# Performance work log

Hardware: AMD Instinct MI355X
Metric: run time of the kernel (lower is better)

Reference implementation:

```python
import jax, jax.numpy as jnp
import numpy as np

DIM = 512
NUM_HEADS = 8
HEAD_DIM = DIM // NUM_HEADS
KERNEL = (3, 5, 5)  # (kd, kh, kw), must be odd and <= spatial dims
B, D, H, W = 1, 6, 48, 96


def setup_inputs() -> dict:
    key = jax.random.key(0)
    ks = jax.random.split(key, 5)
    x = jax.random.normal(ks[0], (B, D, H, W, DIM), jnp.float32)
    w_qkv = jax.random.normal(ks[1], (DIM, 3 * DIM), jnp.float32) * 0.02
    b_qkv = jax.random.normal(ks[2], (3 * DIM,), jnp.float32) * 0.02
    w_proj = jax.random.normal(ks[3], (DIM, DIM), jnp.float32) * 0.02
    b_proj = jax.random.normal(ks[4], (DIM,), jnp.float32) * 0.02
    return {"x": x, "w_qkv": w_qkv, "b_qkv": b_qkv, "w_proj": w_proj, "b_proj": b_proj}


def _nbhd_idx(L, k):
    # NATTEN neighborhood: window of exactly k keys, centered, shifted inward at edges.
    p = jnp.arange(L)
    start = jnp.clip(p - k // 2, 0, L - k)
    return start[:, None] + jnp.arange(k)[None, :]  # [L, k]


def _na3d(q, k, v, kernel):
    # q, k, v: [B, D, H, W, heads, hd]; q pre-scaled.
    kd, kh, kw = kernel
    _, Dd, Hh, Ww, _, _ = q.shape
    idx_d = _nbhd_idx(Dd, kd)
    idx_h = _nbhd_idx(Hh, kh)
    idx_w = _nbhd_idx(Ww, kw)
    offs = jnp.stack(
        jnp.meshgrid(jnp.arange(kd), jnp.arange(kh), jnp.arange(kw), indexing="ij"),
        axis=-1,
    ).reshape(-1, 3)  # [K3, 3]

    def shift(t, o):
        # gather the o-th neighbor of every query position along each spatial axis
        t = jnp.take(t, jnp.take(idx_d, o[0], axis=1), axis=1)
        t = jnp.take(t, jnp.take(idx_h, o[1], axis=1), axis=2)
        t = jnp.take(t, jnp.take(idx_w, o[2], axis=1), axis=3)
        return t

    def score_step(_, o):
        k_s = shift(k, o)
        s = jnp.einsum("bdhwnc,bdhwnc->bdhwn", q, k_s)
        return None, s

    _, scores = jax.lax.scan(score_step, None, offs)  # [K3, B, D, H, W, heads]
    attn = jax.nn.softmax(scores, axis=0)

    def out_step(acc, xs):
        o, a = xs
        v_s = shift(v, o)
        return acc + a[..., None] * v_s, None

    out, _ = jax.lax.scan(out_step, jnp.zeros_like(q), (offs, attn))
    return out


def reference(x, w_qkv, b_qkv, w_proj, b_proj):
    Bb, Dd, Hh, Ww, C = x.shape
    qkv = (x @ w_qkv + b_qkv).reshape(Bb, Dd, Hh, Ww, 3, NUM_HEADS, HEAD_DIM)
    q = qkv[..., 0, :, :]
    k = qkv[..., 1, :, :]
    v = qkv[..., 2, :, :]
    scale = HEAD_DIM ** (-0.5)
    # Faithful to source: module scales q by self.scale, then tuned_na3d applies
    # head_dim**-0.5 again inside the fused kernel -> net q * head_dim**-1.
    q = q * (scale * scale)
    out = _na3d(q, k, v, KERNEL).reshape(Bb, Dd, Hh, Ww, C)
    return out @ w_proj + b_proj
```

## Files before the change

kernel.cpp:

```cpp
#include <hip/hip_runtime.h>

#define DIMC   512
#define NHEADS 8
#define HDIM   64
#define DD     6
#define HHH    48
#define WWW    96
#define NPOS   (DD * HHH * WWW)

typedef unsigned short u16;
typedef __attribute__((ext_vector_type(8))) short bf16x8;
typedef __attribute__((ext_vector_type(4))) float f32x4;

static __device__ __forceinline__ float b2f(u16 u) {
    return __builtin_bit_cast(float, (unsigned)u << 16);
}
static __device__ __forceinline__ u16 f2b(float f) {
    unsigned x = __builtin_bit_cast(unsigned, f);
    return (u16)((x + 0x7fffu + ((x >> 16) & 1u)) >> 16);
}

static __device__ __forceinline__ void gload_lds16(const void* g, void* l) {
    __builtin_amdgcn_global_load_lds((const __attribute__((address_space(1))) void*)g,
                                     (__attribute__((address_space(3))) void*)l, 16, 0, 0);
}

__global__ __launch_bounds__(256) void cvt_all(
    const float* __restrict__ x, const float* __restrict__ w_qkv,
    const float* __restrict__ w_proj, u16* __restrict__ xb,
    u16* __restrict__ wqkvT, u16* __restrict__ wprojT)
{
    const int bid = blockIdx.x;
    const int tid = threadIdx.x;
    if (bid < 13824) {
        const int i = bid * 256 + tid;
        float4 v = reinterpret_cast<const float4*>(x)[i];
        ushort4 o = { f2b(v.x), f2b(v.y), f2b(v.z), f2b(v.w) };
        reinterpret_cast<ushort4*>(xb)[i] = o;
    } else if (bid < 13824 + 3072) {
        const int id = (bid - 13824) * 256 + tid;
        const int nn = id >> 9, kk = id & 511;
        wqkvT[id] = f2b(w_qkv[(size_t)kk * 1536 + nn]);
    } else {
        const int id = (bid - 16896) * 256 + tid;
        const int nn = id >> 9, kk = id & 511;
        wprojT[id] = f2b(w_proj[(size_t)kk * 512 + nn]);
    }
}

__global__ __launch_bounds__(512) void gemm_bf16_mfma(
    const u16* __restrict__ A, int lda,
    const u16* __restrict__ B, int ldb,
    const float* __restrict__ bias, int Kp,
    void* __restrict__ Cout, int ldc, int cmode, int nx)
{
    __shared__ u16 As[256 * 64];
    __shared__ u16 Bs[128 * 64];

    const int tid = threadIdx.x;
    const int l   = tid & 63;
    const int w   = tid >> 6;
    const int wr  = w >> 1;
    const int wc  = w & 1;

    const int cpx = gridDim.x >> 3;
    const int idp = (blockIdx.x & 7) * cpx + (blockIdx.x >> 3);
    const int by  = idp / nx;
    const int bx  = idp - by * nx;
    const int m0  = by * 256;
    const int n0  = bx * 128;

    const int lrow = l >> 3;
    const int swz  = ((l & 7) ^ lrow) * 8;
    const int arow = w * 32 + lrow;
    const int brow = w * 16 + lrow;

    const u16* ga = A + (size_t)(m0 + arow) * lda + swz;
    const u16* gb = B + (size_t)(n0 + brow) * ldb + swz;
    const size_t a8 = (size_t)8 * lda;
    const size_t b8 = (size_t)8 * ldb;
    u16* const la0 = As + w * 2048;
    u16* const lb0 = Bs + w * 1024;

    f32x4 acc[4][4];
#pragma unroll
    for (int i = 0; i < 4; i++)
#pragma unroll
        for (int j = 0; j < 4; j++) acc[i][j] = (f32x4)0.0f;

    const int c   = l & 15;
    const int g   = l >> 4;
    const int lk0 = ((0 * 4 + g) ^ (c & 7)) * 8;
    const int lk1 = ((1 * 4 + g) ^ (c & 7)) * 8;

#pragma unroll 1
    for (int k0 = 0; k0 < Kp; k0 += 64) {
#pragma unroll
        for (int q = 0; q < 4; ++q)
            gload_lds16(ga + q * a8, la0 + q * 512);
#pragma unroll
        for (int q = 0; q < 2; ++q)
            gload_lds16(gb + q * b8, lb0 + q * 512);
        ga += 64; gb += 64;
        __syncthreads();

        {
            bf16x8 af[4], bfr[4];
#pragma unroll
            for (int f = 0; f < 4; f++) {
                af[f]  = *reinterpret_cast<const bf16x8*>(&As[(wr * 64 + f * 16 + c) * 64 + lk0]);
                bfr[f] = *reinterpret_cast<const bf16x8*>(&Bs[(wc * 64 + f * 16 + c) * 64 + lk0]);
            }
#pragma unroll
            for (int i = 0; i < 4; i++)
#pragma unroll
                for (int j = 0; j < 4; j++)
                    acc[i][j] = __builtin_amdgcn_mfma_f32_16x16x32_bf16(af[i], bfr[j], acc[i][j], 0, 0, 0);
        }
        {
            bf16x8 af[4], bfr[4];
#pragma unroll
            for (int f = 0; f < 4; f++) {
                af[f]  = *reinterpret_cast<const bf16x8*>(&As[(wr * 64 + f * 16 + c) * 64 + lk1]);
                bfr[f] = *reinterpret_cast<const bf16x8*>(&Bs[(wc * 64 + f * 16 + c) * 64 + lk1]);
            }
#pragma unroll
            for (int i = 0; i < 4; i++)
#pragma unroll
                for (int j = 0; j < 4; j++)
                    acc[i][j] = __builtin_amdgcn_mfma_f32_16x16x32_bf16(af[i], bfr[j], acc[i][j], 0, 0, 0);
        }
        __syncthreads();
    }

#pragma unroll
    for (int i = 0; i < 4; i++) {
        const int mb = m0 + wr * 64 + i * 16 + g * 4;
#pragma unroll
        for (int j = 0; j < 4; j++) {
            const int n = n0 + wc * 64 + j * 16 + c;
            const float bv = bias[n];
            const float scn = (cmode && n < 512) ? 0.022542110f : 1.0f;
#pragma unroll
            for (int r = 0; r < 4; r++) {
                const float v = (acc[i][j][r] + bv) * scn;
                if (cmode) reinterpret_cast<u16*>(Cout)[(size_t)(mb + r) * ldc + n] = f2b(v);
                else       reinterpret_cast<float*>(Cout)[(size_t)(mb + r) * ldc + n] = v;
            }
        }
    }
}

__global__ __launch_bounds__(512, 4) void na3d_mfma(
    const u16* __restrict__ qkv, u16* __restrict__ attnc)
{
    __shared__ int   rowoff[192];
    __shared__ int   dlt[16];
    __shared__ u16   Vt[NHEADS][64][36];
    __shared__ float ssum_lds[NHEADS][16];

    const int bid = blockIdx.x;
    const int x   = bid & 7;
    const int u   = bid >> 3;
    const int twl = u / 72;
    const int r2  = u - twl * 72;
    const int pd  = r2 / 12;
    const int thp = r2 - pd * 12;
    const int h0  = thp * 4;
    const int w0  = (3 * x + twl) * 4;
    const int sd  = min(max(pd - 1, 0), DD - 3);
    const int shb = min(max(h0 - 2, 0), HHH - 5);
    const int swb = min(max(w0 - 2, 0), WWW - 5);

    const int tid = threadIdx.x;
    if (tid < 192) {
        const int dd = tid >> 6, hh = (tid >> 3) & 7, wu = tid & 7;
        const int row = (sd + dd) * (HHH * WWW)
                      + min(shb + hh, HHH - 1) * WWW + min(swb + wu, WWW - 1);
        rowoff[tid] = row * 1536;
    }
    if (tid < 16) {
        const int ph = h0 + (tid >> 2), pw = w0 + (tid & 3);
        const int dh = min(max(ph - 2, 0), HHH - 5) - shb;
        const int dw = min(max(pw - 2, 0), WWW - 5) - swb;
        dlt[tid] = (dh << 4) | dw;
    }
    __syncthreads();

    const int head = tid >> 6;
    const int l    = tid & 63;
    const int g    = l >> 4;
    const int c    = l & 15;

    const int qrowi = pd * (HHH * WWW) + (h0 + (c >> 2)) * WWW + (w0 + (c & 3));
    const u16* qrow = qkv + (size_t)qrowi * 1536 + head * HDIM;
    const bf16x8 qlo = *reinterpret_cast<const bf16x8*>(qrow + 8 * g);
    const bf16x8 qhi = *reinterpret_cast<const bf16x8*>(qrow + 32 + 8 * g);
    const int dparts = dlt[c];
    const int dh = dparts >> 4, dw = dparts & 15;

    f32x4 oacc[4];
#pragma unroll
    for (int j = 0; j < 4; j++) oacc[j] = (f32x4)0.0f;
    float ssum = 0.0f;

#pragma unroll 1
    for (int s = 0; s < 6; ++s) {
        {
            const int npair = l >> 2;
            const int chq   = l & 3;
#pragma unroll
            for (int rr = 0; rr < 2; ++rr) {
                const int ch8 = 8 * chq + 32 * rr;
                const int2 rp = *reinterpret_cast<const int2*>(&rowoff[s * 32 + 2 * npair]);
                const ushort4* pa = reinterpret_cast<const ushort4*>(qkv + rp.x + 1024 + head * HDIM + ch8);
                const ushort4* pb = reinterpret_cast<const ushort4*>(qkv + rp.y + 1024 + head * HDIM + ch8);
                ushort4 va0 = pa[0], va1 = pa[1];
                ushort4 vb0 = pb[0], vb1 = pb[1];
                const u16* va = reinterpret_cast<const u16*>(&va0);
                const u16* vb = reinterpret_cast<const u16*>(&vb0);
#pragma unroll
                for (int e = 0; e < 4; ++e) {
                    unsigned dwo = (unsigned)va[e] | ((unsigned)vb[e] << 16);
                    *reinterpret_cast<unsigned*>(&Vt[head][ch8 + e][2 * npair]) = dwo;
                }
                const u16* va2 = reinterpret_cast<const u16*>(&va1);
                const u16* vb2 = reinterpret_cast<const u16*>(&vb1);
#pragma unroll
                for (int e = 0; e < 4; ++e) {
                    unsigned dwo = (unsigned)va2[e] | ((unsigned)vb2[e] << 16);
                    *reinterpret_cast<unsigned*>(&Vt[head][ch8 + 4 + e][2 * npair]) = dwo;
                }
            }
        }

        unsigned pA, pB, pC, pD;
#pragma unroll
        for (int t = 0; t < 2; ++t) {
            const int sb0 = s * 32 + t * 16;
            const int ro  = rowoff[sb0 + c];
            const u16* kr = qkv + ro + 512 + head * HDIM;
            const bf16x8 klo = *reinterpret_cast<const bf16x8*>(kr + 8 * g);
            const bf16x8 khi = *reinterpret_cast<const bf16x8*>(kr + 32 + 8 * g);
            f32x4 sf = (f32x4)0.0f;
            sf = __builtin_amdgcn_mfma_f32_16x16x32_bf16(klo, qlo, sf, 0, 0, 0);
            sf = __builtin_amdgcn_mfma_f32_16x16x32_bf16(khi, qhi, sf, 0, 0, 0);
            const int sb  = sb0 + 4 * g;
            const int wu0 = sb & 7;
            const int hh_ = (sb >> 3) & 7;
            const bool hv = ((unsigned)(hh_ - dh) < 5u);
            float e0, e1, e2, e3;
            e0 = (hv && (unsigned)(wu0 + 0 - dw) < 5u) ? exp2f(sf[0]) : 0.0f;
            e1 = (hv && (unsigned)(wu0 + 1 - dw) < 5u) ? exp2f(sf[1]) : 0.0f;
            e2 = (hv && (unsigned)(wu0 + 2 - dw) < 5u) ? exp2f(sf[2]) : 0.0f;
            e3 = (hv && (unsigned)(wu0 + 3 - dw) < 5u) ? exp2f(sf[3]) : 0.0f;
            ssum += e0 + e1 + e2 + e3;
            const unsigned p01 = (unsigned)f2b(e0) | ((unsigned)f2b(e1) << 16);
            const unsigned p23 = (unsigned)f2b(e2) | ((unsigned)f2b(e3) << 16);
            if (t == 0) { pA = p01; pB = p23; }
            else        { pC = p01; pD = p23; }
        }

        asm volatile("v_permlane32_swap_b32 %0, %1" : "+v"(pA), "+v"(pC));
        asm volatile("v_permlane32_swap_b32 %0, %1" : "+v"(pB), "+v"(pD));
        asm volatile("v_permlane16_swap_b32 %0, %1" : "+v"(pA), "+v"(pC));
        asm volatile("v_permlane16_swap_b32 %0, %1" : "+v"(pB), "+v"(pD));

        {
            const int4 pv = make_int4((int)pA, (int)pB, (int)pC, (int)pD);
            const bf16x8 pfrag = __builtin_bit_cast(bf16x8, pv);
#pragma unroll
            for (int j = 0; j < 4; ++j) {
                const uint2 v01 = *reinterpret_cast<const uint2*>(&Vt[head][16 * j + c][8 * g]);
                const uint2 v23 = *reinterpret_cast<const uint2*>(&Vt[head][16 * j + c][8 * g + 4]);
                const int4 vv = make_int4((int)v01.x, (int)v01.y, (int)v23.x, (int)v23.y);
                const bf16x8 vfrag = __builtin_bit_cast(bf16x8, vv);
                oacc[j] = __builtin_amdgcn_mfma_f32_16x16x32_bf16(pfrag, vfrag, oacc[j], 0, 0, 0);
            }
        }
    }

    ssum += __shfl_xor(ssum, 16);
    ssum += __shfl_xor(ssum, 32);
    if (l < 16) ssum_lds[head][c] = ssum;
    const f32x4 sums4 = *reinterpret_cast<const f32x4*>(&ssum_lds[head][4 * g]);

    const int orow = pd * (HHH * WWW) + (h0 + g) * WWW + w0;
#pragma unroll
    for (int r = 0; r < 4; ++r) {
        const float inv = 1.0f / sums4[r];
        u16* base = attnc + (size_t)(orow + r) * 512 + head * HDIM;
#pragma unroll
        for (int j = 0; j < 4; ++j)
            base[16 * j + c] = f2b(oacc[j][r] * inv);
    }
}

extern "C" void kernel_launch(void* const* d_in, const int* in_sizes, int n_in,
                              void* d_out, int out_size, void* d_ws, size_t ws_size,
                              hipStream_t stream)
{
    const float* x      = (const float*)d_in[0];
    const float* w_qkv  = (const float*)d_in[1];
    const float* b_qkv  = (const float*)d_in[2];
    const float* w_proj = (const float*)d_in[3];
    const float* b_proj = (const float*)d_in[4];
    float* out = (float*)d_out;

    u16* qkvb   = (u16*)d_ws;
    u16* attnc  = qkvb  + (size_t)NPOS * 1536;
    u16* xb     = attnc + (size_t)NPOS * 512;
    u16* wqkvT  = xb    + (size_t)NPOS * 512;
    u16* wprojT = wqkvT + (size_t)1536 * 512;

    cvt_all<<<17920, 256, 0, stream>>>(x, w_qkv, w_proj, xb, wqkvT, wprojT);

    gemm_bf16_mfma<<<(NPOS / 256) * (1536 / 128), 512, 0, stream>>>(
        xb, 512, wqkvT, 512, b_qkv, 512, qkvb, 1536, 1, 1536 / 128);

    na3d_mfma<<<NPOS / 16, 512, 0, stream>>>(qkvb, attnc);

    gemm_bf16_mfma<<<(NPOS / 256) * (512 / 128), 512, 0, stream>>>(
        attnc, 512, wprojT, 512, b_proj, 512, out, 512, 0, 512 / 128);
}
```

Before: 162.1 us.

## Process two depth slices per attention block to share K/V neighborhood loads

Each neighborhood-attention block now handles a 4x4 query tile across two adjacent depth slices. It loads a 4-deep K/V halo once and applies per-slice depth masks, where before each block loaded a 3-deep halo for a single slice. This cuts redundant K/V global loads and V transposes into LDS per output, and halves the grid size. In exchange each block does more MFMA work per loaded tile, computes some masked-out scores, and holds more accumulator registers, which may lower occupancy.

```diff
diff --git a/kernel.cpp b/kernel.cpp
--- a/kernel.cpp
+++ b/kernel.cpp
@@ -154,28 +154,30 @@
 __global__ __launch_bounds__(512, 4) void na3d_mfma(
     const u16* __restrict__ qkv, u16* __restrict__ attnc)
 {
-    __shared__ int   rowoff[192];
+    __shared__ int   rowoff[256];
     __shared__ int   dlt[16];
     __shared__ u16   Vt[NHEADS][64][36];
-    __shared__ float ssum_lds[NHEADS][16];
+    __shared__ float ssum_lds[NHEADS][2][16];
 
     const int bid = blockIdx.x;
     const int x   = bid & 7;
     const int u   = bid >> 3;
-    const int twl = u / 72;
-    const int r2  = u - twl * 72;
-    const int pd  = r2 / 12;
-    const int thp = r2 - pd * 12;
+    const int twl = u / 36;
+    const int r2  = u - twl * 36;
+    const int d0  = r2 / 12;
+    const int thp = r2 - d0 * 12;
     const int h0  = thp * 4;
     const int w0  = (3 * x + twl) * 4;
-    const int sd  = min(max(pd - 1, 0), DD - 3);
+    const int sdu = min(max(2 * d0 - 1, 0), DD - 4);
     const int shb = min(max(h0 - 2, 0), HHH - 5);
     const int swb = min(max(w0 - 2, 0), WWW - 5);
+    const int ddlt0 = min(max(2 * d0 - 1, 0), DD - 3) - sdu;
+    const int ddlt1 = min(max(2 * d0, 0), DD - 3) - sdu;
 
     const int tid = threadIdx.x;
-    if (tid < 192) {
+    if (tid < 256) {
         const int dd = tid >> 6, hh = (tid >> 3) & 7, wu = tid & 7;
-        const int row = (sd + dd) * (HHH * WWW)
+        const int row = (sdu + dd) * (HHH * WWW)
                       + min(shb + hh, HHH - 1) * WWW + min(swb + wu, WWW - 1);
         rowoff[tid] = row * 1536;
     }
@@ -192,20 +194,23 @@
     const int g    = l >> 4;
     const int c    = l & 15;
 
-    const int qrowi = pd * (HHH * WWW) + (h0 + (c >> 2)) * WWW + (w0 + (c & 3));
-    const u16* qrow = qkv + (size_t)qrowi * 1536 + head * HDIM;
-    const bf16x8 qlo = *reinterpret_cast<const bf16x8*>(qrow + 8 * g);
-    const bf16x8 qhi = *reinterpret_cast<const bf16x8*>(qrow + 32 + 8 * g);
+    const int qbase = (h0 + (c >> 2)) * WWW + (w0 + (c & 3));
+    const u16* qrow0 = qkv + (size_t)((2 * d0)     * (HHH * WWW) + qbase) * 1536 + head * HDIM;
+    const u16* qrow1 = qkv + (size_t)((2 * d0 + 1) * (HHH * WWW) + qbase) * 1536 + head * HDIM;
+    const bf16x8 qlo0 = *reinterpret_cast<const bf16x8*>(qrow0 + 8 * g);
+    const bf16x8 qhi0 = *reinterpret_cast<const bf16x8*>(qrow0 + 32 + 8 * g);
+    const bf16x8 qlo1 = *reinterpret_cast<const bf16x8*>(qrow1 + 8 * g);
+    const bf16x8 qhi1 = *reinterpret_cast<const bf16x8*>(qrow1 + 32 + 8 * g);
     const int dparts = dlt[c];
     const int dh = dparts >> 4, dw = dparts & 15;
 
-    f32x4 oacc[4];
-#pragma unroll
-    for (int j = 0; j < 4; j++) oacc[j] = (f32x4)0.0f;
-    float ssum = 0.0f;
+    f32x4 oacc0[4], oacc1[4];
+#pragma unroll
+    for (int j = 0; j < 4; j++) { oacc0[j] = (f32x4)0.0f; oacc1[j] = (f32x4)0.0f; }
+    float ssum0 = 0.0f, ssum1 = 0.0f;
 
 #pragma unroll 1
-    for (int s = 0; s < 6; ++s) {
+    for (int s = 0; s < 8; ++s) {
         {
             const int npair = l >> 2;
             const int chq   = l & 3;
@@ -234,65 +239,105 @@
             }
         }
 
-        unsigned pA, pB, pC, pD;
-#pragma unroll
-        for (int t = 0; t < 2; ++t) {
-            const int sb0 = s * 32 + t * 16;
-            const int ro  = rowoff[sb0 + c];
+        f32x4 sf00 = (f32x4)0.0f, sf01 = (f32x4)0.0f;
+        f32x4 sf10 = (f32x4)0.0f, sf11 = (f32x4)0.0f;
+        {
+            const int ro = rowoff[s * 32 + c];
             const u16* kr = qkv + ro + 512 + head * HDIM;
             const bf16x8 klo = *reinterpret_cast<const bf16x8*>(kr + 8 * g);
             const bf16x8 khi = *reinterpret_cast<const bf16x8*>(kr + 32 + 8 * g);
-            f32x4 sf = (f32x4)0.0f;
-            sf = __builtin_amdgcn_mfma_f32_16x16x32_bf16(klo, qlo, sf, 0, 0, 0);
-            sf = __builtin_amdgcn_mfma_f32_16x16x32_bf16(khi, qhi, sf, 0, 0, 0);
-            const int sb  = sb0 + 4 * g;
-            const int wu0 = sb & 7;
-            const int hh_ = (sb >> 3) & 7;
-            const bool hv = ((unsigned)(hh_ - dh) < 5u);
-            float e0, e1, e2, e3;
-            e0 = (hv && (unsigned)(wu0 + 0 - dw) < 5u) ? exp2f(sf[0]) : 0.0f;
-            e1 = (hv && (unsigned)(wu0 + 1 - dw) < 5u) ? exp2f(sf[1]) : 0.0f;
-            e2 = (hv && (unsigned)(wu0 + 2 - dw) < 5u) ? exp2f(sf[2]) : 0.0f;
-            e3 = (hv && (unsigned)(wu0 + 3 - dw) < 5u) ? exp2f(sf[3]) : 0.0f;
-            ssum += e0 + e1 + e2 + e3;
-            const unsigned p01 = (unsigned)f2b(e0) | ((unsigned)f2b(e1) << 16);
-            const unsigned p23 = (unsigned)f2b(e2) | ((unsigned)f2b(e3) << 16);
-            if (t == 0) { pA = p01; pB = p23; }
-            else        { pC = p01; pD = p23; }
-        }
-
-        asm volatile("v_permlane32_swap_b32 %0, %1" : "+v"(pA), "+v"(pC));
-        asm volatile("v_permlane32_swap_b32 %0, %1" : "+v"(pB), "+v"(pD));
-        asm volatile("v_permlane16_swap_b32 %0, %1" : "+v"(pA), "+v"(pC));
-        asm volatile("v_permlane16_swap_b32 %0, %1" : "+v"(pB), "+v"(pD));
-
-        {
-            const int4 pv = make_int4((int)pA, (int)pB, (int)pC, (int)pD);
-            const bf16x8 pfrag = __builtin_bit_cast(bf16x8, pv);
+            sf00 = __builtin_amdgcn_mfma_f32_16x16x32_bf16(klo, qlo0, sf00, 0, 0, 0);
+            sf00 = __builtin_amdgcn_mfma_f32_16x16x32_bf16(khi, qhi0, sf00, 0, 0, 0);
+            sf01 = __builtin_amdgcn_mfma_f32_16x16x32_bf16(klo, qlo1, sf01, 0, 0, 0);
+            sf01 = __builtin_amdgcn_mfma_f32_16x16x32_bf16(khi, qhi1, sf01, 0, 0, 0);
+        }
+        {
+            const int ro = rowoff[s * 32 + 16 + c];
+            const u16* kr = qkv + ro + 512 + head * HDIM;
+            const bf16x8 klo = *reinterpret_cast<const bf16x8*>(kr + 8 * g);
+            const bf16x8 khi = *reinterpret_cast<const bf16x8*>(kr + 32 + 8 * g);
+            sf10 = __builtin_amdgcn_mfma_f32_16x16x32_bf16(klo, qlo0, sf10, 0, 0, 0);
+            sf10 = __builtin_amdgcn_mfma_f32_16x16x32_bf16(khi, qhi0, sf10, 0, 0, 0);
+            sf11 = __builtin_amdgcn_mfma_f32_16x16x32_bf16(klo, qlo1, sf11, 0, 0, 0);
+            sf11 = __builtin_amdgcn_mfma_f32_16x16x32_bf16(khi, qhi1, sf11, 0, 0, 0);
+        }
+
+        const int sbA  = s * 32 + 4 * g;
+        const int sbB  = sbA + 16;
+        const int ddA  = sbA >> 6, hhA = (sbA >> 3) & 7, wuA = sbA & 7;
+        const int ddB  = sbB >> 6, hhB = (sbB >> 3) & 7, wuB = sbB & 7;
+        const bool hvA = ((unsigned)(hhA - dh) < 5u);
+        const bool hvB = ((unsigned)(hhB - dh) < 5u);
+
+        unsigned pA0, pB0, pC0, pD0, pA1, pB1, pC1, pD1;
+#define EXPPACK(sf, dvA_, pX, pY, SSUM, hv_, wu_) do {                          \
+    const bool v_ = (dvA_) && (hv_);                                            \
+    const float e0 = (v_ && (unsigned)((wu_) + 0 - dw) < 5u) ? exp2f((sf)[0]) : 0.0f; \
+    const float e1 = (v_ && (unsigned)((wu_) + 1 - dw) < 5u) ? exp2f((sf)[1]) : 0.0f; \
+    const float e2 = (v_ && (unsigned)((wu_) + 2 - dw) < 5u) ? exp2f((sf)[2]) : 0.0f; \
+    const float e3 = (v_ && (unsigned)((wu_) + 3 - dw) < 5u) ? exp2f((sf)[3]) : 0.0f; \
+    SSUM += e0 + e1 + e2 + e3;                                                  \
+    pX = (unsigned)f2b(e0) | ((unsigned)f2b(e1) << 16);                         \
+    pY = (unsigned)f2b(e2) | ((unsigned)f2b(e3) << 16);                         \
+} while (0)
+
+        EXPPACK(sf00, ((unsigned)(ddA - ddlt0) < 3u), pA0, pB0, ssum0, hvA, wuA);
+        EXPPACK(sf10, ((unsigned)(ddB - ddlt0) < 3u), pC0, pD0, ssum0, hvB, wuB);
+        EXPPACK(sf01, ((unsigned)(ddA - ddlt1) < 3u), pA1, pB1, ssum1, hvA, wuA);
+        EXPPACK(sf11, ((unsigned)(ddB - ddlt1) < 3u), pC1, pD1, ssum1, hvB, wuB);
+#undef EXPPACK
+
+        asm volatile("v_permlane32_swap_b32 %0, %1" : "+v"(pA0), "+v"(pC0));
+        asm volatile("v_permlane32_swap_b32 %0, %1" : "+v"(pB0), "+v"(pD0));
+        asm volatile("v_permlane16_swap_b32 %0, %1" : "+v"(pA0), "+v"(pC0));
+        asm volatile("v_permlane16_swap_b32 %0, %1" : "+v"(pB0), "+v"(pD0));
+        asm volatile("v_permlane32_swap_b32 %0, %1" : "+v"(pA1), "+v"(pC1));
+        asm volatile("v_permlane32_swap_b32 %0, %1" : "+v"(pB1), "+v"(pD1));
+        asm volatile("v_permlane16_swap_b32 %0, %1" : "+v"(pA1), "+v"(pC1));
+        asm volatile("v_permlane16_swap_b32 %0, %1" : "+v"(pB1), "+v"(pD1));
+
+        {
+            const bf16x8 pf0 = __builtin_bit_cast(bf16x8,
+                make_int4((int)pA0, (int)pB0, (int)pC0, (int)pD0));
+            const bf16x8 pf1 = __builtin_bit_cast(bf16x8,
+                make_int4((int)pA1, (int)pB1, (int)pC1, (int)pD1));
 #pragma unroll
             for (int j = 0; j < 4; ++j) {
                 const uint2 v01 = *reinterpret_cast<const uint2*>(&Vt[head][16 * j + c][8 * g]);
                 const uint2 v23 = *reinterpret_cast<const uint2*>(&Vt[head][16 * j + c][8 * g + 4]);
-                const int4 vv = make_int4((int)v01.x, (int)v01.y, (int)v23.x, (int)v23.y);
-                const bf16x8 vfrag = __builtin_bit_cast(bf16x8, vv);
-                oacc[j] = __builtin_amdgcn_mfma_f32_16x16x32_bf16(pfrag, vfrag, oacc[j], 0, 0, 0);
-            }
-        }
-    }
-
-    ssum += __shfl_xor(ssum, 16);
-    ssum += __shfl_xor(ssum, 32);
-    if (l < 16) ssum_lds[head][c] = ssum;
-    const f32x4 sums4 = *reinterpret_cast<const f32x4*>(&ssum_lds[head][4 * g]);
-
-    const int orow = pd * (HHH * WWW) + (h0 + g) * WWW + w0;
+                const bf16x8 vfrag = __builtin_bit_cast(bf16x8,
+                    make_int4((int)v01.x, (int)v01.y, (int)v23.x, (int)v23.y));
+                oacc0[j] = __builtin_amdgcn_mfma_f32_16x16x32_bf16(pf0, vfrag, oacc0[j], 0, 0, 0);
+                oacc1[j] = __builtin_amdgcn_mfma_f32_16x16x32_bf16(pf1, vfrag, oacc1[j], 0, 0, 0);
+            }
+        }
+    }
+
+    ssum0 += __shfl_xor(ssum0, 16);
+    ssum0 += __shfl_xor(ssum0, 32);
+    ssum1 += __shfl_xor(ssum1, 16);
+    ssum1 += __shfl_xor(ssum1, 32);
+    if (l < 16) {
+        ssum_lds[head][0][c] = ssum0;
+        ssum_lds[head][1][c] = ssum1;
+    }
+    const f32x4 sums40 = *reinterpret_cast<const f32x4*>(&ssum_lds[head][0][4 * g]);
+    const f32x4 sums41 = *reinterpret_cast<const f32x4*>(&ssum_lds[head][1][4 * g]);
+
+    const int obase = (h0 + g) * WWW + w0;
+    const int orow0 = (2 * d0)     * (HHH * WWW) + obase;
+    const int orow1 = (2 * d0 + 1) * (HHH * WWW) + obase;
 #pragma unroll
     for (int r = 0; r < 4; ++r) {
-        const float inv = 1.0f / sums4[r];
-        u16* base = attnc + (size_t)(orow + r) * 512 + head * HDIM;
-#pragma unroll
-        for (int j = 0; j < 4; ++j)
-            base[16 * j + c] = f2b(oacc[j][r] * inv);
+        const float inv0 = 1.0f / sums40[r];
+        const float inv1 = 1.0f / sums41[r];
+        u16* base0 = attnc + (size_t)(orow0 + r) * 512 + head * HDIM;
+        u16* base1 = attnc + (size_t)(orow1 + r) * 512 + head * HDIM;
+#pragma unroll
+        for (int j = 0; j < 4; ++j) {
+            base0[16 * j + c] = f2b(oacc0[j][r] * inv0);
+            base1[16 * j + c] = f2b(oacc1[j][r] * inv1);
+        }
     }
 }
 
@@ -318,7 +363,7 @@
     gemm_bf16_mfma<<<(NPOS / 256) * (1536 / 128), 512, 0, stream>>>(
         xb, 512, wqkvT, 512, b_qkv, 512, qkvb, 1536, 1, 1536 / 128);
 
-    na3d_mfma<<<NPOS / 16, 512, 0, stream>>>(qkvb, attnc);
+    na3d_mfma<<<NPOS / 32, 512, 0, stream>>>(qkvb, attnc);
 
     gemm_bf16_mfma<<<(NPOS / 256) * (512 / 128), 512, 0, stream>>>(
         attnc, 512, wprojT, 512, b_proj, 512, out, 512, 0, 512 / 128);
```

Result: faster. 154.0 us, median of 4 (-5.0%).
